# Kernel tuning notes

Measured on AMD Instinct MI355X. Metric: run time of the kernel, lower is better.

## Reference

```python
import jax, jax.numpy as jnp
import numpy as np

B, S, I, H, O = 32, 1024, 128, 1024, 64
SPECTRAL_RADIUS = 0.9


def setup_inputs() -> dict:
    key = jax.random.key(0)
    k_x, k_w, k_win, k_wo, k_bo = jax.random.split(key, 5)
    x = jax.random.normal(k_x, (B, S, I), dtype=jnp.float32)
    # Reservoir matrix: uniform[-0.5, 0.5], rescaled so spectral radius = 0.9
    w = np.asarray(jax.random.uniform(k_w, (H, H), dtype=jnp.float32)) - 0.5
    max_eig = np.abs(np.linalg.eigvals(w.astype(np.float64))).max().astype(np.float32)
    W_res = jnp.asarray(w * (SPECTRAL_RADIUS / max_eig), dtype=jnp.float32)
    W_in = jax.random.uniform(k_win, (H, I), dtype=jnp.float32) - 0.5
    # Readout (nn.Linear) params
    lim = 1.0 / np.sqrt(H)
    W_out_w = jax.random.uniform(k_wo, (O, H), minval=-lim, maxval=lim, dtype=jnp.float32)
    W_out_b = jax.random.uniform(k_bo, (O,), minval=-lim, maxval=lim, dtype=jnp.float32)
    return {"x": x, "W_res": W_res, "W_in": W_in, "W_out_w": W_out_w, "W_out_b": W_out_b}


def reference(x, W_res, W_in, W_out_w, W_out_b):
    # x: [B, S, I] -> scan over time with hidden state h: [B, H]
    xs = jnp.swapaxes(x, 0, 1)  # [S, B, I]
    h0 = jnp.zeros((x.shape[0], W_res.shape[0]), dtype=x.dtype)

    def step(h, u):
        h = jnp.tanh(h @ W_res.T + u @ W_in.T)
        return h, h

    _, hs = jax.lax.scan(step, h0, xs)  # hs: [S, B, H]
    # per-step linear readout, batched over all steps (same math as in-loop readout)
    out = jnp.einsum('sbh,oh->sbo', hs, W_out_w) + W_out_b  # [S, B, O]
    return jnp.swapaxes(out, 0, 1)  # [B, S, O]
```

## Files before the change

### kernel.cpp

```cpp
#include <hip/hip_runtime.h>
#include <cmath>

#define NB 32
#define NS 1024
#define NI 128
#define NH 1024
#define NO 64


__device__ __forceinline__ float load_llc(const float* p) {
    float v;
    asm volatile("global_load_dword %0, %1, off sc0 sc1" : "=v"(v) : "v"(p));
    return v;
}

extern "C" __global__ void __launch_bounds__(256, 1)
esn_persistent(const float* __restrict__ x,
               const float* __restrict__ W_res,
               const float* __restrict__ W_in,
               const float* __restrict__ W_out_w,
               const float* __restrict__ W_out_b,
               float* __restrict__ out,
               unsigned char* ws)
{
    const int tid  = threadIdx.x;
    const int lane = tid & 63;
    const int wv   = tid >> 6;
    const int bg   = (int)blockIdx.x & 7;
    const int rs   = (int)blockIdx.x >> 3;
    const int rt   = tid & 7;
    const int kid  = tid >> 3;
    const int r0   = rs * 32 + rt * 4;
    const int k0   = kid * 32;
    const int o0   = rs * 2;

    unsigned int* cnt = (unsigned int*)ws + bg * 32;
    float* h_buf = (float*)(ws + 4096);

    __shared__ float4 h4[1055];
    __shared__ float4 xl4[128];
    __shared__ float4 redA[4 * 8 * 4];
    __shared__ float  red2[4][8][2][4];

    float w_r[4][32];
#pragma unroll
    for (int rr = 0; rr < 4; ++rr) {
        const float* wp = W_res + (r0 + rr) * NH + k0;
#pragma unroll
        for (int q = 0; q < 8; ++q) {
            float4 v = *(const float4*)(wp + q * 4);
            w_r[rr][q * 4 + 0] = v.x;
            w_r[rr][q * 4 + 1] = v.y;
            w_r[rr][q * 4 + 2] = v.z;
            w_r[rr][q * 4 + 3] = v.w;
        }
    }
    float4 w_i[4];
#pragma unroll
    for (int rr = 0; rr < 4; ++rr)
        w_i[rr] = *(const float4*)(W_in + (r0 + rr) * NI + kid * 4);
    float w_o[2][4];
#pragma unroll
    for (int it = 0; it < 4; ++it) {
        w_o[0][it] = W_out_w[(o0 + 0) * NH + tid + it * 256];
        w_o[1][it] = W_out_w[(o0 + 1) * NH + tid + it * 256];
    }
    const float bias = W_out_b[o0 + ((tid >> 2) & 1)];

    const float* xrow = x + ((bg * 4 + (tid >> 6)) * NS) * NI + (tid & 63) * 2;
    float* outb = out + (bg * 4) * (NS * NO);

    float2 xstash = *(const float2*)(xrow);

    for (int s = 0; s < NS; ++s) {
        ((float2*)xl4)[(tid >> 6) * 64 + (tid & 63)] = xstash;
        __syncthreads();
        {
            int sn = (s + 1 < NS) ? s + 1 : s;
            xstash = *(const float2*)(xrow + sn * NI);
        }

        float acc[4][4];
#pragma unroll
        for (int rr = 0; rr < 4; ++rr)
#pragma unroll
            for (int bb = 0; bb < 4; ++bb) acc[rr][bb] = 0.f;

        {
            float4 xv[4];
#pragma unroll
            for (int bb = 0; bb < 4; ++bb) xv[bb] = xl4[bb * 32 + kid];
#pragma unroll
            for (int rr = 0; rr < 4; ++rr) {
#pragma unroll
                for (int bb = 0; bb < 4; ++bb) {
                    float v = acc[rr][bb];
                    v = fmaf(w_i[rr].x, xv[bb].x, v);
                    v = fmaf(w_i[rr].y, xv[bb].y, v);
                    v = fmaf(w_i[rr].z, xv[bb].z, v);
                    v = fmaf(w_i[rr].w, xv[bb].w, v);
                    acc[rr][bb] = v;
                }
            }
        }
        if (s != 0) {
            const float4* hp = &h4[k0 + kid];
#pragma unroll
            for (int kk = 0; kk < 32; ++kk) {
                float4 hv = hp[kk];
#pragma unroll
                for (int rr = 0; rr < 4; ++rr) {
                    float w = w_r[rr][kk];
                    acc[rr][0] = fmaf(w, hv.x, acc[rr][0]);
                    acc[rr][1] = fmaf(w, hv.y, acc[rr][1]);
                    acc[rr][2] = fmaf(w, hv.z, acc[rr][2]);
                    acc[rr][3] = fmaf(w, hv.w, acc[rr][3]);
                }
            }
        }
#pragma unroll
        for (int rr = 0; rr < 4; ++rr)
#pragma unroll
            for (int bb = 0; bb < 4; ++bb) {
                float v = acc[rr][bb];
                v += __shfl_xor(v, 8, 64);
                v += __shfl_xor(v, 16, 64);
                v += __shfl_xor(v, 32, 64);
                acc[rr][bb] = v;
            }
        if ((lane & 56) == 0) {
#pragma unroll
            for (int rr = 0; rr < 4; ++rr)
                redA[(wv * 8 + rt) * 4 + rr] =
                    make_float4(acc[rr][0], acc[rr][1], acc[rr][2], acc[rr][3]);
        }
        __syncthreads();
        const int hsel = s & 1;
        if (tid < 128) {
            const int rl = tid & 31;
            const int bb = tid >> 5;
            const float* redF = (const float*)redA;
            const int base = ((rl >> 2) * 4 + (rl & 3)) * 4 + bb;
            float v = redF[base] + redF[128 + base] + redF[256 + base] + redF[384 + base];
            v = tanhf(v);
            __hip_atomic_store(
                &h_buf[hsel * (NB * NH) + (bg * 4 + bb) * NH + rs * 32 + rl],
                v, __ATOMIC_RELAXED, __HIP_MEMORY_SCOPE_AGENT);
            asm volatile("s_waitcnt vmcnt(0)" ::: "memory");
        }
        __syncthreads();
        if (tid == 0) {
            __hip_atomic_fetch_add(cnt, 1u, __ATOMIC_RELAXED,
                                   __HIP_MEMORY_SCOPE_AGENT);
            const unsigned target = 32u * (unsigned)(s + 1);
            while (__hip_atomic_load(cnt, __ATOMIC_RELAXED,
                                     __HIP_MEMORY_SCOPE_AGENT) < target) {}
        }
        __syncthreads();
        __builtin_amdgcn_sched_barrier(0);

        const float* hb = h_buf + hsel * (NB * NH) + (bg * 4) * NH;
        float hv[4][4];
#pragma unroll
        for (int it = 0; it < 4; ++it) {
            const int k = tid + it * 256;
#pragma unroll
            for (int bb = 0; bb < 4; ++bb)
                hv[it][bb] = load_llc(hb + bb * NH + k);
        }
        asm volatile("s_waitcnt vmcnt(0)" ::: "memory");
        __builtin_amdgcn_sched_barrier(0);

        float ro[2][4] = {{0.f, 0.f, 0.f, 0.f}, {0.f, 0.f, 0.f, 0.f}};
#pragma unroll
        for (int it = 0; it < 4; ++it) {
            const int k = tid + it * 256;
            h4[k + (k >> 5)] = make_float4(hv[it][0], hv[it][1], hv[it][2], hv[it][3]);
#pragma unroll
            for (int o = 0; o < 2; ++o)
#pragma unroll
                for (int bb = 0; bb < 4; ++bb)
                    ro[o][bb] = fmaf(w_o[o][it], hv[it][bb], ro[o][bb]);
        }
#pragma unroll
        for (int o = 0; o < 2; ++o)
#pragma unroll
            for (int bb = 0; bb < 4; ++bb) {
                float v = ro[o][bb];
                v += __shfl_xor(v, 1, 64);
                v += __shfl_xor(v, 2, 64);
                v += __shfl_xor(v, 4, 64);
                ro[o][bb] = v;
            }
        if ((lane & 7) == 0) {
#pragma unroll
            for (int o = 0; o < 2; ++o)
#pragma unroll
                for (int bb = 0; bb < 4; ++bb)
                    red2[wv][lane >> 3][o][bb] = ro[o][bb];
        }
        __syncthreads();
        if (tid < 8) {
            const int o  = tid >> 2;
            const int bb = tid & 3;
            float v = bias;
#pragma unroll
            for (int ww = 0; ww < 4; ++ww)
#pragma unroll
                for (int g = 0; g < 8; ++g)
                    v += red2[ww][g][o][bb];
            outb[bb * (NS * NO) + s * NO + o0 + o] = v;
        }
    }
}

extern "C" void kernel_launch(void* const* d_in, const int* in_sizes, int n_in,
                              void* d_out, int out_size, void* d_ws, size_t ws_size,
                              hipStream_t stream)
{
    const float* x       = (const float*)d_in[0];
    const float* W_res   = (const float*)d_in[1];
    const float* W_in    = (const float*)d_in[2];
    const float* W_out_w = (const float*)d_in[3];
    const float* W_out_b = (const float*)d_in[4];
    float* out           = (float*)d_out;
    unsigned char* ws    = (unsigned char*)d_ws;

    hipMemsetAsync(d_ws, 0, 4096, stream);

    void* args[] = {&x, &W_res, &W_in, &W_out_w, &W_out_b, &out, &ws};
    hipError_t err = hipLaunchCooperativeKernel((void*)esn_persistent,
                                                dim3(256), dim3(256),
                                                args, 0, stream);
    if (err != hipSuccess) {
        (void)hipGetLastError();
        hipLaunchKernelGGL(esn_persistent, dim3(256), dim3(256), 0, stream,
                           x, W_res, W_in, W_out_w, W_out_b, out, ws);
    }
}
```

Measured before the change: 5.185 ms.

## Replace atomic counter barrier with per-block flags and vectorized hidden-state exchange

Swaps the per-group atomic counter barrier for per-producer flag words. Each block publishes its step number, and each thread polls only the one producer block whose hidden slice it needs, so there is no shared atomic and no extra block-wide sync. The hidden state is now stored batch-interleaved as float4 (all 4 batches per hidden unit), so producers write and consumers read with dwordx4 LLC-coherent accesses instead of scalar ones. This cuts memory transactions and counter contention on the critical path of the sequential recurrence. The cost is that every thread spins on global memory, which adds polling traffic, and correctness now depends on the store ordering of the inline asm.

```diff
diff --git a/kernel.cpp b/kernel.cpp
--- a/kernel.cpp
+++ b/kernel.cpp
@@ -7,10 +7,25 @@
 #define NH 1024
 #define NO 64
 
-
-__device__ __forceinline__ float load_llc(const float* p) {
-    float v;
-    asm volatile("global_load_dword %0, %1, off sc0 sc1" : "=v"(v) : "v"(p));
+typedef float f32x4 __attribute__((ext_vector_type(4)));
+typedef float f32x2 __attribute__((ext_vector_type(2)));
+
+
+__device__ __forceinline__ void store_llc4(f32x4* p, f32x4 v) {
+    asm volatile("global_store_dwordx4 %0, %1, off sc0 sc1" :: "v"(p), "v"(v) : "memory");
+}
+__device__ __forceinline__ f32x4 load_llc4(const f32x4* p) {
+    f32x4 v;
+    asm volatile("global_load_dwordx4 %0, %1, off sc0 sc1" : "=v"(v) : "v"(p));
+    return v;
+}
+__device__ __forceinline__ void store_llc_u32(unsigned* p, unsigned v) {
+    asm volatile("global_store_dword %0, %1, off sc0 sc1" :: "v"(p), "v"(v) : "memory");
+}
+__device__ __forceinline__ unsigned poll_llc_u32(const unsigned* p) {
+    unsigned v;
+    asm volatile("global_load_dword %0, %1, off sc0 sc1\n\ts_waitcnt vmcnt(0)"
+                 : "=v"(v) : "v"(p) : "memory");
     return v;
 }
 
@@ -33,51 +48,54 @@
     const int r0   = rs * 32 + rt * 4;
     const int k0   = kid * 32;
     const int o0   = rs * 2;
-
-    unsigned int* cnt = (unsigned int*)ws + bg * 32;
-    float* h_buf = (float*)(ws + 4096);
-
-    __shared__ float4 h4[1055];
-    __shared__ float4 xl4[128];
-    __shared__ float4 redA[4 * 8 * 4];
-    __shared__ float  red2[4][8][2][4];
+    const int p    = tid >> 3;
+    const int q    = tid & 7;
+
+    unsigned* flags = (unsigned*)ws;
+    f32x4* h_buf4   = (f32x4*)(ws + 4096);
+
+    __shared__ f32x4 h4[1055];
+    __shared__ f32x4 xl4[128];
+    __shared__ f32x4 redA[128];
+    __shared__ float red2[4][8][2][4];
 
     float w_r[4][32];
 #pragma unroll
     for (int rr = 0; rr < 4; ++rr) {
         const float* wp = W_res + (r0 + rr) * NH + k0;
 #pragma unroll
-        for (int q = 0; q < 8; ++q) {
-            float4 v = *(const float4*)(wp + q * 4);
-            w_r[rr][q * 4 + 0] = v.x;
-            w_r[rr][q * 4 + 1] = v.y;
-            w_r[rr][q * 4 + 2] = v.z;
-            w_r[rr][q * 4 + 3] = v.w;
-        }
-    }
-    float4 w_i[4];
+        for (int qq = 0; qq < 8; ++qq) {
+            f32x4 v = *(const f32x4*)(wp + qq * 4);
+            w_r[rr][qq * 4 + 0] = v.x;
+            w_r[rr][qq * 4 + 1] = v.y;
+            w_r[rr][qq * 4 + 2] = v.z;
+            w_r[rr][qq * 4 + 3] = v.w;
+        }
+    }
+    f32x4 w_i[4];
 #pragma unroll
     for (int rr = 0; rr < 4; ++rr)
-        w_i[rr] = *(const float4*)(W_in + (r0 + rr) * NI + kid * 4);
+        w_i[rr] = *(const f32x4*)(W_in + (r0 + rr) * NI + kid * 4);
     float w_o[2][4];
 #pragma unroll
-    for (int it = 0; it < 4; ++it) {
-        w_o[0][it] = W_out_w[(o0 + 0) * NH + tid + it * 256];
-        w_o[1][it] = W_out_w[(o0 + 1) * NH + tid + it * 256];
+    for (int j = 0; j < 4; ++j) {
+        const int hr = p * 32 + q * 4 + j;
+        w_o[0][j] = W_out_w[(o0 + 0) * NH + hr];
+        w_o[1][j] = W_out_w[(o0 + 1) * NH + hr];
     }
     const float bias = W_out_b[o0 + ((tid >> 2) & 1)];
 
-    const float* xrow = x + ((bg * 4 + (tid >> 6)) * NS) * NI + (tid & 63) * 2;
+    const float* xrow = x + ((bg * 4 + wv) * NS) * NI + lane * 2;
     float* outb = out + (bg * 4) * (NS * NO);
 
-    float2 xstash = *(const float2*)(xrow);
+    f32x2 xstash = *(const f32x2*)(xrow);
 
     for (int s = 0; s < NS; ++s) {
-        ((float2*)xl4)[(tid >> 6) * 64 + (tid & 63)] = xstash;
+        ((f32x2*)xl4)[wv * 64 + lane] = xstash;
         __syncthreads();
         {
             int sn = (s + 1 < NS) ? s + 1 : s;
-            xstash = *(const float2*)(xrow + sn * NI);
+            xstash = *(const f32x2*)(xrow + sn * NI);
         }
 
         float acc[4][4];
@@ -87,7 +105,7 @@
             for (int bb = 0; bb < 4; ++bb) acc[rr][bb] = 0.f;
 
         {
-            float4 xv[4];
+            f32x4 xv[4];
 #pragma unroll
             for (int bb = 0; bb < 4; ++bb) xv[bb] = xl4[bb * 32 + kid];
 #pragma unroll
@@ -104,10 +122,10 @@
             }
         }
         if (s != 0) {
-            const float4* hp = &h4[k0 + kid];
+            const f32x4* hp = &h4[k0 + kid];
 #pragma unroll
             for (int kk = 0; kk < 32; ++kk) {
-                float4 hv = hp[kk];
+                f32x4 hv = hp[kk];
 #pragma unroll
                 for (int rr = 0; rr < 4; ++rr) {
                     float w = w_r[rr][kk];
@@ -130,57 +148,55 @@
             }
         if ((lane & 56) == 0) {
 #pragma unroll
-            for (int rr = 0; rr < 4; ++rr)
-                redA[(wv * 8 + rt) * 4 + rr] =
-                    make_float4(acc[rr][0], acc[rr][1], acc[rr][2], acc[rr][3]);
+            for (int rr = 0; rr < 4; ++rr) {
+                f32x4 t = {acc[rr][0], acc[rr][1], acc[rr][2], acc[rr][3]};
+                redA[(wv * 8 + rt) * 4 + rr] = t;
+            }
         }
         __syncthreads();
         const int hsel = s & 1;
-        if (tid < 128) {
-            const int rl = tid & 31;
-            const int bb = tid >> 5;
-            const float* redF = (const float*)redA;
-            const int base = ((rl >> 2) * 4 + (rl & 3)) * 4 + bb;
-            float v = redF[base] + redF[128 + base] + redF[256 + base] + redF[384 + base];
-            v = tanhf(v);
-            __hip_atomic_store(
-                &h_buf[hsel * (NB * NH) + (bg * 4 + bb) * NH + rs * 32 + rl],
-                v, __ATOMIC_RELAXED, __HIP_MEMORY_SCOPE_AGENT);
+        f32x4* hb4s = h_buf4 + hsel * 8192 + bg * 1024 + rs * 32;
+        if (tid < 32) {
+            const int rt2 = tid >> 2, rr2 = tid & 3;
+            f32x4 v = redA[(0 * 8 + rt2) * 4 + rr2] + redA[(1 * 8 + rt2) * 4 + rr2]
+                    + redA[(2 * 8 + rt2) * 4 + rr2] + redA[(3 * 8 + rt2) * 4 + rr2];
+            v.x = tanhf(v.x); v.y = tanhf(v.y); v.z = tanhf(v.z); v.w = tanhf(v.w);
+            store_llc4(hb4s + tid, v);
             asm volatile("s_waitcnt vmcnt(0)" ::: "memory");
         }
         __syncthreads();
-        if (tid == 0) {
-            __hip_atomic_fetch_add(cnt, 1u, __ATOMIC_RELAXED,
-                                   __HIP_MEMORY_SCOPE_AGENT);
-            const unsigned target = 32u * (unsigned)(s + 1);
-            while (__hip_atomic_load(cnt, __ATOMIC_RELAXED,
-                                     __HIP_MEMORY_SCOPE_AGENT) < target) {}
-        }
-        __syncthreads();
+        if (tid == 0) store_llc_u32(flags + (bg * 32 + rs) * 2, (unsigned)(s + 1));
+
+        {
+            const unsigned tgt = (unsigned)(s + 1);
+            const unsigned* fp = flags + (bg * 32 + p) * 2;
+            while (poll_llc_u32(fp) < tgt) {}
+        }
         __builtin_amdgcn_sched_barrier(0);
-
-        const float* hb = h_buf + hsel * (NB * NH) + (bg * 4) * NH;
-        float hv[4][4];
-#pragma unroll
-        for (int it = 0; it < 4; ++it) {
-            const int k = tid + it * 256;
-#pragma unroll
-            for (int bb = 0; bb < 4; ++bb)
-                hv[it][bb] = load_llc(hb + bb * NH + k);
-        }
+        const f32x4* hb4 = h_buf4 + hsel * 8192 + bg * 1024 + p * 32 + q * 4;
+        f32x4 hv0 = load_llc4(hb4 + 0);
+        f32x4 hv1 = load_llc4(hb4 + 1);
+        f32x4 hv2 = load_llc4(hb4 + 2);
+        f32x4 hv3 = load_llc4(hb4 + 3);
         asm volatile("s_waitcnt vmcnt(0)" ::: "memory");
         __builtin_amdgcn_sched_barrier(0);
 
-        float ro[2][4] = {{0.f, 0.f, 0.f, 0.f}, {0.f, 0.f, 0.f, 0.f}};
-#pragma unroll
-        for (int it = 0; it < 4; ++it) {
-            const int k = tid + it * 256;
-            h4[k + (k >> 5)] = make_float4(hv[it][0], hv[it][1], hv[it][2], hv[it][3]);
-#pragma unroll
-            for (int o = 0; o < 2; ++o)
-#pragma unroll
-                for (int bb = 0; bb < 4; ++bb)
-                    ro[o][bb] = fmaf(w_o[o][it], hv[it][bb], ro[o][bb]);
+        {
+            const int base = p * 33 + q * 4;
+            h4[base + 0] = hv0; h4[base + 1] = hv1;
+            h4[base + 2] = hv2; h4[base + 3] = hv3;
+        }
+        float ro[2][4];
+#pragma unroll
+        for (int o = 0; o < 2; ++o) {
+            ro[o][0] = fmaf(w_o[o][0], hv0.x, fmaf(w_o[o][1], hv1.x,
+                       fmaf(w_o[o][2], hv2.x, w_o[o][3] * hv3.x)));
+            ro[o][1] = fmaf(w_o[o][0], hv0.y, fmaf(w_o[o][1], hv1.y,
+                       fmaf(w_o[o][2], hv2.y, w_o[o][3] * hv3.y)));
+            ro[o][2] = fmaf(w_o[o][0], hv0.z, fmaf(w_o[o][1], hv1.z,
+                       fmaf(w_o[o][2], hv2.z, w_o[o][3] * hv3.z)));
+            ro[o][3] = fmaf(w_o[o][0], hv0.w, fmaf(w_o[o][1], hv1.w,
+                       fmaf(w_o[o][2], hv2.w, w_o[o][3] * hv3.w)));
         }
 #pragma unroll
         for (int o = 0; o < 2; ++o)
```

New measurement: 7.675 ms. 48.0% more time.
